# Optimization experiments

Hardware: AMD Instinct MI355X
Metric: run time of the kernel (lower is better)

## Reference

```python
import jax, jax.numpy as jnp
import numpy as np

HEADS = 4


def setup_inputs() -> dict:
    key = jax.random.key(0)
    ks = jax.random.split(key, 5)
    B, T, C, H, W = 2, 16, 256, 64, 64
    x = jax.random.normal(ks[0], (B, T, C, H, W), dtype=jnp.float32)
    s = 1.0 / np.sqrt(C).astype(np.float32)  # kaiming-ish init scale for 1x1 conv
    Wq = jax.random.normal(ks[1], (C, C), dtype=jnp.float32) * s
    Wk = jax.random.normal(ks[2], (C, C), dtype=jnp.float32) * s
    Wv = jax.random.normal(ks[3], (C, C), dtype=jnp.float32) * s
    Wp = jax.random.normal(ks[4], (C, C), dtype=jnp.float32) * s
    return {"x": x, "Wq": Wq, "Wk": Wk, "Wv": Wv, "Wp": Wp}


def reference(x, Wq, Wk, Wv, Wp):
    B, T, C, H, W = x.shape
    heads = HEADS
    Ch = C // heads
    scale = Ch ** (-0.5)
    # [B,T,C,H,W] -> [B*H*W, T, C]: each spatial pixel has a T x C temporal track
    xf = jnp.transpose(x, (0, 3, 4, 1, 2)).reshape(B * H * W, T, C)
    # Conv1d(C,C,1,bias=False) == channel matmul: out[n,t,d] = sum_c W[d,c] x[n,t,c]
    q = jnp.einsum('ntc,dc->ntd', xf, Wq).reshape(-1, T, heads, Ch) * scale
    k = jnp.einsum('ntc,dc->ntd', xf, Wk).reshape(-1, T, heads, Ch)
    v = jnp.einsum('ntc,dc->ntd', xf, Wv).reshape(-1, T, heads, Ch)
    k_soft = jax.nn.softmax(k, axis=1)    # softmax over time T (torch dim=-1 of [n,h,c,t])
    q_soft = jax.nn.softmax(q, axis=-1)   # softmax over head channels Ch (torch dim=-2)
    # linear attention: outer-product context then query contraction
    kv = jnp.einsum('nthc,nthd->nhcd', k_soft, v)         # [N,h,Ch,Ch]
    out = jnp.einsum('nthc,nhcd->nthd', q_soft, kv)       # [N,T,h,Ch]
    out = out.reshape(-1, T, C)
    out = jnp.einsum('ntc,dc->ntd', out, Wp)
    out = out.reshape(B, H, W, T, C)
    return jnp.transpose(out, (0, 3, 4, 1, 2))
```

## Files before the change

kernel.cpp:

```cpp
#include <hip/hip_runtime.h>
#include <hip/hip_bf16.h>

#define DI __device__ __forceinline__

typedef __attribute__((ext_vector_type(8))) short bf16x8;
typedef __attribute__((ext_vector_type(4))) float f32x4;
typedef __attribute__((ext_vector_type(4))) _Float16 f16x4;

constexpr int XPAD = 264;
constexpr float LOG2E = 1.4426950408889634f;

DI float fexp(float x) { return __builtin_amdgcn_exp2f(x * LOG2E); }
DI float frcp(float x) { return __builtin_amdgcn_rcpf(x); }

DI short f2bf(float f) {
  __hip_bfloat16 h = __float2bfloat16(f);
  union { __hip_bfloat16 h; short s; } c; c.h = h; return c.s;
}

DI unsigned pk2(float a, float b) {
  union { __hip_bfloat162 h; unsigned u; } c;
  c.h.x = __float2bfloat16(a); c.h.y = __float2bfloat16(b);
  return c.u;
}

DI short f2h(float f) {
  _Float16 h = (_Float16)f;
  union { _Float16 h; short s; } c; c.h = h; return c.s;
}

DI f16x4 pkh4(float a, float b, float c, float d) {
  auto lo = __builtin_amdgcn_cvt_pkrtz(a, b);
  auto hi = __builtin_amdgcn_cvt_pkrtz(c, d);
  union { struct { decltype(lo) l, h; } p; f16x4 v; } u;
  u.p.l = lo; u.p.h = hi;
  return u.v;
}

DI f16x4 ld4h(const short* p) {
  union { uint2 u; f16x4 v; } c;
  c.u = *(const uint2*)p;
  return c.v;
}

DI f32x4 mfma16(bf16x8 a, bf16x8 b, f32x4 c) {
  return __builtin_amdgcn_mfma_f32_16x16x32_bf16(a, b, c, 0, 0, 0);
}

DI f32x4 mfmah(f16x4 a, f16x4 b, f32x4 c) {
  return __builtin_amdgcn_mfma_f32_16x16x16f16(a, b, c, 0, 0, 0);
}

DI f32x4 fzero() { return f32x4{0.f, 0.f, 0.f, 0.f}; }

DI int xsw(int row, int e) { return row * 256 + (e ^ ((row & 7) << 3)); }

__global__ void wconv_kernel(const float* __restrict__ a, const float* __restrict__ b,
                             const float* __restrict__ c, const float* __restrict__ d,
                             short* __restrict__ o) {
  int i = blockIdx.x * 256 + threadIdx.x;
  int mat = i >> 14;
  int off = (i & 16383) * 4;
  const float* s = (mat == 0) ? a : (mat == 1) ? b : (mat == 2) ? c : d;
  const float sc = (mat == 0) ? 0.125f : 1.0f;
  float4 v = *(const float4*)(s + off);
  uint2 r; r.x = pk2(v.x * sc, v.y * sc); r.y = pk2(v.z * sc, v.w * sc);
  *(uint2*)(o + mat * 65536 + off) = r;
}

__global__ __launch_bounds__(256, 2)
void xt_kernel(const float* __restrict__ x, short* __restrict__ xt, int n0chunk) {
  __shared__ short T[64 * 258];
  const int tid = threadIdx.x;
  const int gi  = blockIdx.x >> 4;
  const int t   = blockIdx.x & 15;
  const int n0g = n0chunk + gi * 64;
  const int b   = n0g >> 12;
  const int hw0 = n0g & 4095;
  const float* xb = x + ((size_t)(b * 16 + t) * 256) * 4096 + hw0;

  #pragma unroll
  for (int ci = 0; ci < 16; ++ci) {
    const int c   = ci * 16 + (tid >> 4);
    const int px4 = tid & 15;
    float4 v = *(const float4*)(xb + (size_t)c * 4096 + px4 * 4);
    T[(px4 * 4 + 0) * 258 + c] = f2bf(v.x);
    T[(px4 * 4 + 1) * 258 + c] = f2bf(v.y);
    T[(px4 * 4 + 2) * 258 + c] = f2bf(v.z);
    T[(px4 * 4 + 3) * 258 + c] = f2bf(v.w);
  }
  __syncthreads();

  const int wave = tid >> 6, lane = tid & 63;
  #pragma unroll
  for (int itp = 0; itp < 16; ++itp) {
    const int px  = itp * 4 + wave;
    const int row = (px & 3) * 16 + t;
    const int sw8 = (row & 7) << 3;
    const size_t obase = ((size_t)(gi * 16 + (px >> 2))) * 16384 + row * 256;
    const int dstc = (((lane >> 1) * 8) ^ sw8) + (lane & 1) * 4;
    const int tb = px * 258 + lane * 4;
    union { short s[4]; uint2 u; } pk;
    pk.s[0] = T[tb + 0]; pk.s[1] = T[tb + 1];
    pk.s[2] = T[tb + 2]; pk.s[3] = T[tb + 3];
    *(uint2*)&xt[obase + dstc] = pk.u;
  }
}

__global__ __launch_bounds__(256, 4)
void k1_kernel(const short* __restrict__ xt, const short* __restrict__ wbf,
               short* __restrict__ att, short* __restrict__ qsg) {
  __shared__ short SMEM[16384];
  short* Xs = SMEM;

  const int tid  = threadIdx.x;
  const int wave = tid >> 6;
  const int lane = tid & 63;
  const int g    = lane >> 4;
  const int li   = lane & 15;

  int bid = blockIdx.x;
  const int nb = gridDim.x;
  if ((nb & 7) == 0) { const int q = nb >> 3; bid = (bid & 7) * q + (bid >> 3); }

  {
    const short* src = xt + (size_t)bid * 16384 + wave * 512 + lane * 8;
    #pragma unroll
    for (int it = 0; it < 8; ++it) {
      __builtin_amdgcn_global_load_lds(
          (const __attribute__((address_space(1))) void*)(src + it * 2048),
          (__attribute__((address_space(3))) void*)(SMEM + it * 2048 + wave * 512),
          16, 0, 0);
    }
  }
  __syncthreads();

  const short* wq = wbf;
  const short* wk = wbf + 65536;
  const short* wv = wbf + 131072;
  const size_t wrow = (size_t)(wave * 64) * 256;
  short* qsw = qsg + ((size_t)bid * 4 * 4 + wave) * 1024;

  {
    f32x4 qacc[4][4];
    #pragma unroll
    for (int p = 0; p < 4; ++p)
      #pragma unroll
      for (int nt = 0; nt < 4; ++nt) qacc[p][nt] = fzero();

    __builtin_amdgcn_s_setprio(1);
    #pragma unroll
    for (int ks = 0; ks < 8; ++ks) {
      bf16x8 qb[4];
      #pragma unroll
      for (int nt = 0; nt < 4; ++nt)
        qb[nt] = *(const bf16x8*)(wq + wrow + (size_t)(nt * 16 + li) * 256 + ks * 32 + g * 8);
      #pragma unroll
      for (int p = 0; p < 4; ++p) {
        bf16x8 af = *(const bf16x8*)&Xs[xsw(p * 16 + li, ks * 32 + g * 8)];
        #pragma unroll
        for (int nt = 0; nt < 4; ++nt)
          qacc[p][nt] = mfma16(af, qb[nt], qacc[p][nt]);
      }
    }
    __builtin_amdgcn_s_setprio(0);

    #pragma unroll
    for (int p = 0; p < 4; ++p) {
      short* qsp = qsw + p * 4096;
      #pragma unroll
      for (int r = 0; r < 4; ++r) {
        float e0 = fexp(qacc[p][0][r]);
        float e1 = fexp(qacc[p][1][r]);
        float e2 = fexp(qacc[p][2][r]);
        float e3 = fexp(qacc[p][3][r]);
        float s = e0 + e1 + e2 + e3;
        s += __shfl_xor(s, 1); s += __shfl_xor(s, 2);
        s += __shfl_xor(s, 4); s += __shfl_xor(s, 8);
        const float inv = frcp(s);
        const int t = g * 4 + r;
        short* dst = qsp + t * 64 + li;
        dst[0]  = f2h(e0 * inv);
        dst[16] = f2h(e1 * inv);
        dst[32] = f2h(e2 * inv);
        dst[48] = f2h(e3 * inv);
      }
    }
  }

  f16x4 akf[4][4];
  {
    f32x4 kacc[4][4];
    #pragma unroll
    for (int p = 0; p < 4; ++p)
      #pragma unroll
      for (int nt = 0; nt < 4; ++nt) kacc[p][nt] = fzero();

    __builtin_amdgcn_s_setprio(1);
    #pragma unroll
    for (int ks = 0; ks < 8; ++ks) {
      bf16x8 kb[4];
      #pragma unroll
      for (int nt = 0; nt < 4; ++nt)
        kb[nt] = *(const bf16x8*)(wk + wrow + (size_t)(nt * 16 + li) * 256 + ks * 32 + g * 8);
      #pragma unroll
      for (int p = 0; p < 4; ++p) {
        bf16x8 af = *(const bf16x8*)&Xs[xsw(p * 16 + li, ks * 32 + g * 8)];
        #pragma unroll
        for (int nt = 0; nt < 4; ++nt)
          kacc[p][nt] = mfma16(af, kb[nt], kacc[p][nt]);
      }
    }
    __builtin_amdgcn_s_setprio(0);

    #pragma unroll
    for (int p = 0; p < 4; ++p)
      #pragma unroll
      for (int nt = 0; nt < 4; ++nt) {
        float e0 = fexp(kacc[p][nt][0]);
        float e1 = fexp(kacc[p][nt][1]);
        float e2 = fexp(kacc[p][nt][2]);
        float e3 = fexp(kacc[p][nt][3]);
        float s = e0 + e1 + e2 + e3;
        s += __shfl_xor(s, 16);
        s += __shfl_xor(s, 32);
        const float inv = frcp(s);
        akf[p][nt] = pkh4(e0 * inv, e1 * inv, e2 * inv, e3 * inv);
      }
  }

  f16x4 bvf[4][4];
  #pragma unroll
  for (int h = 0; h < 2; ++h) {
    f32x4 vacc[4][2];
    #pragma unroll
    for (int p = 0; p < 4; ++p)
      #pragma unroll
      for (int n2 = 0; n2 < 2; ++n2) vacc[p][n2] = fzero();

    __builtin_amdgcn_s_setprio(1);
    #pragma unroll
    for (int ks = 0; ks < 8; ++ks) {
      bf16x8 vb[2];
      #pragma unroll
      for (int n2 = 0; n2 < 2; ++n2)
        vb[n2] = *(const bf16x8*)(wv + wrow + (size_t)((h * 2 + n2) * 16 + li) * 256 + ks * 32 + g * 8);
      #pragma unroll
      for (int p = 0; p < 4; ++p) {
        bf16x8 af = *(const bf16x8*)&Xs[xsw(p * 16 + li, ks * 32 + g * 8)];
        #pragma unroll
        for (int n2 = 0; n2 < 2; ++n2)
          vacc[p][n2] = mfma16(af, vb[n2], vacc[p][n2]);
      }
    }
    __builtin_amdgcn_s_setprio(0);

    #pragma unroll
    for (int p = 0; p < 4; ++p)
      #pragma unroll
      for (int n2 = 0; n2 < 2; ++n2)
        bvf[p][h * 2 + n2] = pkh4(vacc[p][n2][0], vacc[p][n2][1],
                                  vacc[p][n2][2], vacc[p][n2][3]);
  }

  asm volatile("s_waitcnt vmcnt(0)" ::: "memory");

  #pragma unroll
  for (int p = 0; p < 4; ++p) {
    const short* qsp = qsw + p * 4096;
    f32x4 oacc[4];
    #pragma unroll
    for (int nt = 0; nt < 4; ++nt) oacc[nt] = fzero();

    #pragma unroll
    for (int cq = 0; cq < 4; ++cq) {
      f32x4 kva[4];
      #pragma unroll
      for (int nt = 0; nt < 4; ++nt)
        kva[nt] = mfmah(akf[p][cq], bvf[p][nt], fzero());
      f16x4 aq = ld4h(qsp + li * 64 + cq * 16 + g * 4);
      #pragma unroll
      for (int nt = 0; nt < 4; ++nt) {
        f16x4 kb16 = pkh4(kva[nt][0], kva[nt][1], kva[nt][2], kva[nt][3]);
        oacc[nt] = mfmah(aq, kb16, oacc[nt]);
      }
    }

    const size_t arow = ((size_t)bid * 4 + p) * 16;
    #pragma unroll
    for (int nt = 0; nt < 4; ++nt)
      #pragma unroll
      for (int r = 0; r < 4; ++r)
        att[(arow + g * 4 + r) * 256 + wave * 64 + nt * 16 + li] = f2bf(oacc[nt][r]);
  }
}

__global__ __launch_bounds__(256, 2)
void k2_kernel(const short* __restrict__ att, const short* __restrict__ wpb,
               float* __restrict__ out, int n0chunk) {
  __shared__ short A[128 * XPAD];
  const int tid = threadIdx.x;
  const int wave = tid >> 6, lane = tid & 63, g = lane >> 4, li = lane & 15;
  const int pb = blockIdx.x >> 1;
  const int t0 = (blockIdx.x & 1) * 8;
  const int n0 = n0chunk + pb * 16;
  const int b = n0 >> 12, hw0 = n0 & 4095;

  for (int idx = tid; idx < 128 * 32; idx += 256) {
    const int row = idx >> 5, seg = idx & 31;
    const int p = row & 15, tl = row >> 4;
    const short* src = att + ((size_t)((pb * 16 + p) * 16 + t0 + tl)) * 256 + seg * 8;
    *(int4*)&A[row * XPAD + seg * 8] = *(const int4*)src;
  }
  __syncthreads();

  f32x4 acc[8][4];
  #pragma unroll
  for (int mt = 0; mt < 8; ++mt)
    #pragma unroll
    for (int n4 = 0; n4 < 4; ++n4) acc[mt][n4] = fzero();

  #pragma unroll
  for (int ks = 0; ks < 8; ++ks) {
    bf16x8 bf[4];
    #pragma unroll
    for (int n4 = 0; n4 < 4; ++n4)
      bf[n4] = *(const bf16x8*)(wpb + (size_t)((wave * 4 + n4) * 16 + li) * 256 + ks * 32 + g * 8);
    #pragma unroll
    for (int mt = 0; mt < 8; ++mt) {
      bf16x8 af = *(const bf16x8*)&A[(mt * 16 + li) * XPAD + ks * 32 + g * 8];
      #pragma unroll
      for (int n4 = 0; n4 < 4; ++n4) acc[mt][n4] = mfma16(af, bf[n4], acc[mt][n4]);
    }
  }

  float* ob = out + (size_t)b * (16 * 256 * 4096) + hw0;
  #pragma unroll
  for (int mt = 0; mt < 8; ++mt)
    #pragma unroll
    for (int n4 = 0; n4 < 4; ++n4) {
      const int t = t0 + mt;
      const int c = (wave * 4 + n4) * 16 + li;
      float4 v;
      v.x = acc[mt][n4][0]; v.y = acc[mt][n4][1];
      v.z = acc[mt][n4][2]; v.w = acc[mt][n4][3];
      *(float4*)(ob + (size_t)(t * 256 + c) * 4096 + g * 4) = v;
    }
}

extern "C" void kernel_launch(void* const* d_in, const int* in_sizes, int n_in,
                              void* d_out, int out_size, void* d_ws, size_t ws_size,
                              hipStream_t stream) {
  const float* x  = (const float*)d_in[0];
  const float* Wq = (const float*)d_in[1];
  const float* Wk = (const float*)d_in[2];
  const float* Wv = (const float*)d_in[3];
  const float* Wp = (const float*)d_in[4];
  float* out = (float*)d_out;

  short* wbf = (short*)d_ws;
  short* att = wbf + 4 * 65536;

  wconv_kernel<<<256, 256, 0, stream>>>(Wq, Wk, Wv, Wp, wbf);

  const size_t wsAvail = (ws_size > 524288) ? (ws_size - 524288) : 0;
  const size_t perPix = 16 * 256 * 2;
  int chunk = 64;
  while (chunk < 8192 && (size_t)(chunk * 3) * perPix <= wsAvail) chunk <<= 1;

  short* xtb = att + (size_t)chunk * 4096;
  short* qsg = xtb + (size_t)chunk * 4096;

  for (int n0 = 0; n0 < 8192; n0 += chunk) {
    xt_kernel<<<(chunk / 64) * 16, 256, 0, stream>>>(x, xtb, n0);
    k1_kernel<<<chunk / 4, 256, 0, stream>>>(xtb, wbf, att, qsg);
    k2_kernel<<<(chunk / 16) * 2, 256, 0, stream>>>(att, wbf + 3 * 65536, out, n0);
  }
}
```

Baseline: 252.7 us.

## Split k1 work across 8 waves, each handling half the pixels per head

The k1 kernel now launches 512 threads per block. Each of the 8 waves owns one head and two of the four pixels instead of one head and all four pixels, so per-wave accumulator and fragment arrays are halved. The V projection is done in one pass over four n-tiles instead of two half passes. The aim is lower register pressure and more waves per CU to hide latency. The cost is that each wave reloads the same weight fragments for half as much MFMA work, so weight traffic per unit of compute doubles.

```diff
diff --git a/kernel.cpp b/kernel.cpp
--- a/kernel.cpp
+++ b/kernel.cpp
@@ -107,29 +107,31 @@
   }
 }
 
-__global__ __launch_bounds__(256, 4)
+__global__ __launch_bounds__(512, 4)
 void k1_kernel(const short* __restrict__ xt, const short* __restrict__ wbf,
                short* __restrict__ att, short* __restrict__ qsg) {
   __shared__ short SMEM[16384];
   short* Xs = SMEM;
 
   const int tid  = threadIdx.x;
-  const int wave = tid >> 6;
+  const int wv   = tid >> 6;
   const int lane = tid & 63;
   const int g    = lane >> 4;
   const int li   = lane & 15;
+  const int h    = wv & 3;
+  const int s    = wv >> 2;
 
   int bid = blockIdx.x;
   const int nb = gridDim.x;
   if ((nb & 7) == 0) { const int q = nb >> 3; bid = (bid & 7) * q + (bid >> 3); }
 
   {
-    const short* src = xt + (size_t)bid * 16384 + wave * 512 + lane * 8;
-    #pragma unroll
-    for (int it = 0; it < 8; ++it) {
+    const short* src = xt + (size_t)bid * 16384 + wv * 512 + lane * 8;
+    #pragma unroll
+    for (int it = 0; it < 4; ++it) {
       __builtin_amdgcn_global_load_lds(
-          (const __attribute__((address_space(1))) void*)(src + it * 2048),
-          (__attribute__((address_space(3))) void*)(SMEM + it * 2048 + wave * 512),
+          (const __attribute__((address_space(1))) void*)(src + it * 4096),
+          (__attribute__((address_space(3))) void*)(SMEM + it * 4096 + wv * 512),
           16, 0, 0);
     }
   }
@@ -137,14 +139,13 @@
 
   const short* wq = wbf;
   const short* wk = wbf + 65536;
-  const short* wv = wbf + 131072;
-  const size_t wrow = (size_t)(wave * 64) * 256;
-  short* qsw = qsg + ((size_t)bid * 4 * 4 + wave) * 1024;
+  const short* wv_ = wbf + 131072;
+  const size_t wrow = (size_t)(h * 64) * 256;
 
   {
-    f32x4 qacc[4][4];
-    #pragma unroll
-    for (int p = 0; p < 4; ++p)
+    f32x4 qacc[2][4];
+    #pragma unroll
+    for (int p = 0; p < 2; ++p)
       #pragma unroll
       for (int nt = 0; nt < 4; ++nt) qacc[p][nt] = fzero();
 
@@ -156,8 +157,8 @@
       for (int nt = 0; nt < 4; ++nt)
         qb[nt] = *(const bf16x8*)(wq + wrow + (size_t)(nt * 16 + li) * 256 + ks * 32 + g * 8);
       #pragma unroll
-      for (int p = 0; p < 4; ++p) {
-        bf16x8 af = *(const bf16x8*)&Xs[xsw(p * 16 + li, ks * 32 + g * 8)];
+      for (int p = 0; p < 2; ++p) {
+        bf16x8 af = *(const bf16x8*)&Xs[xsw((2 * s + p) * 16 + li, ks * 32 + g * 8)];
         #pragma unroll
         for (int nt = 0; nt < 4; ++nt)
           qacc[p][nt] = mfma16(af, qb[nt], qacc[p][nt]);
@@ -166,18 +167,18 @@
     __builtin_amdgcn_s_setprio(0);
 
     #pragma unroll
-    for (int p = 0; p < 4; ++p) {
-      short* qsp = qsw + p * 4096;
+    for (int p = 0; p < 2; ++p) {
+      short* qsp = qsg + ((size_t)(bid * 4 + 2 * s + p) * 4 + h) * 1024;
       #pragma unroll
       for (int r = 0; r < 4; ++r) {
         float e0 = fexp(qacc[p][0][r]);
         float e1 = fexp(qacc[p][1][r]);
         float e2 = fexp(qacc[p][2][r]);
         float e3 = fexp(qacc[p][3][r]);
-        float s = e0 + e1 + e2 + e3;
-        s += __shfl_xor(s, 1); s += __shfl_xor(s, 2);
-        s += __shfl_xor(s, 4); s += __shfl_xor(s, 8);
-        const float inv = frcp(s);
+        float sm = e0 + e1 + e2 + e3;
+        sm += __shfl_xor(sm, 1); sm += __shfl_xor(sm, 2);
+        sm += __shfl_xor(sm, 4); sm += __shfl_xor(sm, 8);
+        const float inv = frcp(sm);
         const int t = g * 4 + r;
         short* dst = qsp + t * 64 + li;
         dst[0]  = f2h(e0 * inv);
@@ -188,11 +189,11 @@
     }
   }
 
-  f16x4 akf[4][4];
+  f16x4 akf[2][4];
   {
-    f32x4 kacc[4][4];
-    #pragma unroll
-    for (int p = 0; p < 4; ++p)
+    f32x4 kacc[2][4];
+    #pragma unroll
+    for (int p = 0; p < 2; ++p)
       #pragma unroll
       for (int nt = 0; nt < 4; ++nt) kacc[p][nt] = fzero();
 
@@ -204,8 +205,8 @@
       for (int nt = 0; nt < 4; ++nt)
         kb[nt] = *(const bf16x8*)(wk + wrow + (size_t)(nt * 16 + li) * 256 + ks * 32 + g * 8);
       #pragma unroll
-      for (int p = 0; p < 4; ++p) {
-        bf16x8 af = *(const bf16x8*)&Xs[xsw(p * 16 + li, ks * 32 + g * 8)];
+      for (int p = 0; p < 2; ++p) {
+        bf16x8 af = *(const bf16x8*)&Xs[xsw((2 * s + p) * 16 + li, ks * 32 + g * 8)];
         #pragma unroll
         for (int nt = 0; nt < 4; ++nt)
           kacc[p][nt] = mfma16(af, kb[nt], kacc[p][nt]);
@@ -214,60 +215,59 @@
     __builtin_amdgcn_s_setprio(0);
 
     #pragma unroll
-    for (int p = 0; p < 4; ++p)
+    for (int p = 0; p < 2; ++p)
       #pragma unroll
       for (int nt = 0; nt < 4; ++nt) {
         float e0 = fexp(kacc[p][nt][0]);
         float e1 = fexp(kacc[p][nt][1]);
         float e2 = fexp(kacc[p][nt][2]);
         float e3 = fexp(kacc[p][nt][3]);
-        float s = e0 + e1 + e2 + e3;
-        s += __shfl_xor(s, 16);
-        s += __shfl_xor(s, 32);
-        const float inv = frcp(s);
+        float sm = e0 + e1 + e2 + e3;
+        sm += __shfl_xor(sm, 16);
+        sm += __shfl_xor(sm, 32);
+        const float inv = frcp(sm);
         akf[p][nt] = pkh4(e0 * inv, e1 * inv, e2 * inv, e3 * inv);
       }
   }
 
-  f16x4 bvf[4][4];
-  #pragma unroll
-  for (int h = 0; h < 2; ++h) {
-    f32x4 vacc[4][2];
-    #pragma unroll
-    for (int p = 0; p < 4; ++p)
-      #pragma unroll
-      for (int n2 = 0; n2 < 2; ++n2) vacc[p][n2] = fzero();
+  f16x4 bvf[2][4];
+  {
+    f32x4 vacc[2][4];
+    #pragma unroll
+    for (int p = 0; p < 2; ++p)
+      #pragma unroll
+      for (int nt = 0; nt < 4; ++nt) vacc[p][nt] = fzero();
 
     __builtin_amdgcn_s_setprio(1);
     #pragma unroll
     for (int ks = 0; ks < 8; ++ks) {
-      bf16x8 vb[2];
-      #pragma unroll
-      for (int n2 = 0; n2 < 2; ++n2)
-        vb[n2] = *(const bf16x8*)(wv + wrow + (size_t)((h * 2 + n2) * 16 + li) * 256 + ks * 32 + g * 8);
-      #pragma unroll
-      for (int p = 0; p < 4; ++p) {
-        bf16x8 af = *(const bf16x8*)&Xs[xsw(p * 16 + li, ks * 32 + g * 8)];
+      bf16x8 vb[4];
+      #pragma unroll
+      for (int nt = 0; nt < 4; ++nt)
+        vb[nt] = *(const bf16x8*)(wv_ + wrow + (size_t)(nt * 16 + li) * 256 + ks * 32 + g * 8);
+      #pragma unroll
+      for (int p = 0; p < 2; ++p) {
+        bf16x8 af = *(const bf16x8*)&Xs[xsw((2 * s + p) * 16 + li, ks * 32 + g * 8)];
         #pragma unroll
-        for (int n2 = 0; n2 < 2; ++n2)
-          vacc[p][n2] = mfma16(af, vb[n2], vacc[p][n2]);
+        for (int nt = 0; nt < 4; ++nt)
+          vacc[p][nt] = mfma16(af, vb[nt], vacc[p][nt]);
       }
     }
     __builtin_amdgcn_s_setprio(0);
 
     #pragma unroll
-    for (int p = 0; p < 4; ++p)
-      #pragma unroll
-      for (int n2 = 0; n2 < 2; ++n2)
-        bvf[p][h * 2 + n2] = pkh4(vacc[p][n2][0], vacc[p][n2][1],
-                                  vacc[p][n2][2], vacc[p][n2][3]);
+    for (int p = 0; p < 2; ++p)
+      #pragma unroll
+      for (int nt = 0; nt < 4; ++nt)
+        bvf[p][nt] = pkh4(vacc[p][nt][0], vacc[p][nt][1],
+                          vacc[p][nt][2], vacc[p][nt][3]);
   }
 
   asm volatile("s_waitcnt vmcnt(0)" ::: "memory");
 
   #pragma unroll
-  for (int p = 0; p < 4; ++p) {
-    const short* qsp = qsw + p * 4096;
+  for (int p = 0; p < 2; ++p) {
+    const short* qsp = qsg + ((size_t)(bid * 4 + 2 * s + p) * 4 + h) * 1024;
     f32x4 oacc[4];
     #pragma unroll
     for (int nt = 0; nt < 4; ++nt) oacc[nt] = fzero();
@@ -286,12 +286,12 @@
       }
     }
 
-    const size_t arow = ((size_t)bid * 4 + p) * 16;
+    const size_t arow = ((size_t)bid * 4 + 2 * s + p) * 16;
     #pragma unroll
     for (int nt = 0; nt < 4; ++nt)
       #pragma unroll
       for (int r = 0; r < 4; ++r)
-        att[(arow + g * 4 + r) * 256 + wave * 64 + nt * 16 + li] = f2bf(oacc[nt][r]);
+        att[(arow + g * 4 + r) * 256 + h * 64 + nt * 16 + li] = f2bf(oacc[nt][r]);
   }
 }
 
@@ -373,7 +373,7 @@
 
   for (int n0 = 0; n0 < 8192; n0 += chunk) {
     xt_kernel<<<(chunk / 64) * 16, 256, 0, stream>>>(x, xtb, n0);
-    k1_kernel<<<chunk / 4, 256, 0, stream>>>(xtb, wbf, att, qsg);
+    k1_kernel<<<chunk / 4, 512, 0, stream>>>(xtb, wbf, att, qsg);
     k2_kernel<<<(chunk / 16) * 2, 256, 0, stream>>>(att, wbf + 3 * 65536, out, n0);
   }
 }
```

Result: slower. 326.0 us (+29.0%).
